# Kernel optimization log

Measured on AMD Instinct MI355X. Metric: run time of the kernel, lower is better.

Reference implementation:

```python
import jax, jax.numpy as jnp
import numpy as np
import math

D_EMBED = 128
NUM_HEADS = 4
HEAD_DIM = D_EMBED // NUM_HEADS


def setup_inputs() -> dict:
    key = jax.random.key(0)
    k1, k2, k3 = jax.random.split(key, 3)
    x = jax.random.normal(k1, (4, D_EMBED, 64, 64), dtype=jnp.float32)
    # nn.Linear(d_embed, 3*d_embed): weight [3d, d], bias [3d]; store transposed for x @ W
    scale = 1.0 / math.sqrt(D_EMBED)
    W_qkv = jax.random.uniform(k2, (D_EMBED, 3 * D_EMBED), dtype=jnp.float32, minval=-scale, maxval=scale)
    b_qkv = jax.random.uniform(k3, (3 * D_EMBED,), dtype=jnp.float32, minval=-scale, maxval=scale)
    return {"x": x, "W_qkv": W_qkv, "b_qkv": b_qkv}


def reference(x, W_qkv, b_qkv):
    b, c, h, w = x.shape
    n = h * w
    hd = HEAD_DIM
    # (b, c, h, w) -> (b, n, c) tokens
    t = jnp.transpose(x.reshape(b, c, n), (0, 2, 1))
    qkv = t @ W_qkv + b_qkv  # (b, n, 3c)
    q, k, v = jnp.split(qkv, 3, axis=-1)
    # (b, n, c) -> (b, heads, n, hd)
    def to_heads(u):
        return jnp.transpose(u.reshape(b, n, NUM_HEADS, hd), (0, 2, 1, 3))
    q, k, v = to_heads(q), to_heads(k), to_heads(v)
    # full O(n^2) score matrix, as in the source
    scores = jnp.einsum('bhqd,bhkd->bhqk', q, k) / math.sqrt(hd)
    weights = jax.nn.softmax(scores, axis=-1)
    out = jnp.einsum('bhqk,bhkd->bhqd', weights, v)  # (b, heads, n, hd)
    # permute(0,2,1,3) -> (b, n, heads, hd), then raw reshape to input shape (as in source)
    out = jnp.transpose(out, (0, 2, 1, 3)).reshape(b, c, h, w)
    return out + x
```

## Files before the change

kernel.cpp:

```cpp
#include <hip/hip_runtime.h>
#include <hip/hip_bf16.h>

#define BB 4
#define CC 128
#define NN 4096
#define HH 4
#define HD 32
#define NTOK (BB*NN)

typedef float f32x4 __attribute__((ext_vector_type(4)));
typedef short bf16x8 __attribute__((ext_vector_type(8)));
typedef unsigned short u16;
typedef unsigned int u32;

__device__ __forceinline__ u16 f2bf(float f) {
    union { float f; u32 u; } v; v.f = f;
    u32 r = v.u + 0x7FFF + ((v.u >> 16) & 1);
    return (u16)(r >> 16);
}

__device__ __forceinline__ u32 cvtpk(float lo, float hi) {
    u32 r;
    asm("v_cvt_pk_bf16_f32 %0, %1, %2" : "=v"(r) : "v"(lo), "v"(hi));
    return r;
}

__global__ __launch_bounds__(256) void prep_kernel(const float* __restrict__ x,
                                                   const float* __restrict__ W,
                                                   u16* __restrict__ t_bf,
                                                   u16* __restrict__ Wt_bf) {
    __shared__ u16 tile[64][65];
    int blk = blockIdx.x;
    const float* src; u16* dst; int src_cols, dst_cols, r0, c0;
    if (blk < 512) {
        int b  = blk >> 7;
        int rem = blk & 127;
        int ct = rem >> 6;
        int nt = rem & 63;
        src = x + b * CC * NN;  src_cols = NN; r0 = ct * 64; c0 = nt * 64;
        dst = t_bf + b * NN * CC; dst_cols = CC;
    } else {
        int rem = blk - 512;
        int kt = rem / 6, nt = rem % 6;
        src = W; src_cols = 3 * CC; r0 = kt * 64; c0 = nt * 64;
        dst = Wt_bf; dst_cols = CC;
    }
    int t = threadIdx.x;
#pragma unroll
    for (int p = 0; p < 16; ++p) {
        int rl = p * 4 + (t >> 6);
        int cl = t & 63;
        tile[rl][cl] = f2bf(src[(r0 + rl) * src_cols + c0 + cl]);
    }
    __syncthreads();
#pragma unroll
    for (int p = 0; p < 16; ++p) {
        int cl = p * 4 + (t >> 6);
        int rl = t & 63;
        dst[(c0 + cl) * dst_cols + r0 + rl] = tile[rl][cl];
    }
}

__global__ __launch_bounds__(256, 2) void qkv_gemm(const u16* __restrict__ t_bf,
                                                   const u16* __restrict__ Wt_bf,
                                                   const float* __restrict__ bias,
                                                   u16* __restrict__ Qb,
                                                   u16* __restrict__ Kb,
                                                   u16* __restrict__ Vb) {
    __shared__ u16 Al[128 * 128];
    __shared__ u16 Bl[128 * 128];
    int mt = blockIdx.x;
    int nt = blockIdx.y;
    int t = threadIdx.x;

    {
        const uint4* srcA = (const uint4*)(t_bf + mt * 128 * 128);
        const uint4* srcB = (const uint4*)(Wt_bf + nt * 128 * 128);
#pragma unroll
        for (int p = 0; p < 8; ++p) {
            int cid = p * 256 + t;
            int row = cid >> 4, c16 = cid & 15;
            int sw = (c16 ^ (row & 7)) * 8;
            *(uint4*)(Al + row * 128 + sw) = srcA[cid];
            *(uint4*)(Bl + row * 128 + sw) = srcB[cid];
        }
    }
    __syncthreads();

    int w = t >> 6, l = t & 63;
    int wq = (w >> 1) * 64, wn = (w & 1) * 64;
    int lr = l & 15, lg = l >> 4;

    f32x4 acc[4][4];
#pragma unroll
    for (int mi = 0; mi < 4; ++mi)
#pragma unroll
        for (int ni = 0; ni < 4; ++ni)
            acc[mi][ni] = f32x4{0.f, 0.f, 0.f, 0.f};

#pragma unroll
    for (int kk = 0; kk < 4; ++kk) {
        bf16x8 a[4], bb[4];
        int c = kk * 4 + lg;
#pragma unroll
        for (int mi = 0; mi < 4; ++mi) {
            int R = wq + mi * 16 + lr;
            a[mi] = *(const bf16x8*)(Al + R * 128 + ((c ^ (R & 7)) * 8));
        }
#pragma unroll
        for (int ni = 0; ni < 4; ++ni) {
            int R = wn + ni * 16 + lr;
            bb[ni] = *(const bf16x8*)(Bl + R * 128 + ((c ^ (R & 7)) * 8));
        }
#pragma unroll
        for (int mi = 0; mi < 4; ++mi)
#pragma unroll
            for (int ni = 0; ni < 4; ++ni)
                acc[mi][ni] = __builtin_amdgcn_mfma_f32_16x16x32_bf16(a[mi], bb[ni], acc[mi][ni], 0, 0, 0);
    }

    int b = mt >> 5;
    int tok0 = (mt & 31) * 128 + wq;
    u16* outbuf = (nt == 0) ? Qb : (nt == 1 ? Kb : Vb);
    float qscale = (nt == 0) ? 0.17677669529663687f : 1.0f;
#pragma unroll
    for (int mi = 0; mi < 4; ++mi)
#pragma unroll
        for (int ni = 0; ni < 4; ++ni) {
            int ch = wn + ni * 16 + lr;
            float bv = bias[nt * 128 + ch];
            int hh = ch >> 5, d = ch & 31;
#pragma unroll
            for (int r = 0; r < 4; ++r) {
                int tok = tok0 + mi * 16 + lg * 4 + r;
                float val = (acc[mi][ni][r] + bv) * qscale;
                outbuf[((b * HH + hh) * NN + tok) * HD + d] = f2bf(val);
            }
        }
}

__global__ __launch_bounds__(256) void v_transpose(const u16* __restrict__ Vb,
                                                   u16* __restrict__ Vtb) {
    __shared__ u16 tile[32][65];
    int bh = blockIdx.y;
    int i0 = blockIdx.x * 64;
    int t = threadIdx.x;
    {
        uint4 val = *(const uint4*)(Vb + (bh * NN + i0) * HD + t * 8);
        int row = t >> 2, d8 = (t & 3) * 8;
        u16 tmp[8]; *(uint4*)tmp = val;
#pragma unroll
        for (int j = 0; j < 8; ++j) tile[d8 + j][row] = tmp[j];
    }
    __syncthreads();
    {
        int d = t >> 3, i8 = (t & 7) * 8;
        u16 tmp[8];
#pragma unroll
        for (int j = 0; j < 8; ++j) tmp[j] = tile[d][i8 + j];
        *(uint4*)(Vtb + (bh * HD + d) * NN + i0 + i8) = *(uint4*)tmp;
    }
}

__global__ __launch_bounds__(512, 4) void attn_kernel(const u16* __restrict__ Qb,
                                                      const u16* __restrict__ Kb,
                                                      const u16* __restrict__ Vtb,
                                                      const float* __restrict__ x,
                                                      float* __restrict__ out) {
    __shared__ __align__(16) u16 smem[8192];
    u16* KL = smem;
    u16* VL = smem + 2048;

    int tid = threadIdx.x;
    int w = tid >> 6, l = tid & 63;
    int lr = l & 15, lg = l >> 4;
    int bh = blockIdx.y, b = bh >> 2, hh = bh & 3;
    int q0w = blockIdx.x * 128 + w * 16;

    bf16x8 qa = *(const bf16x8*)(Qb + ((size_t)bh * NN + q0w + lr) * HD + lg * 8);

    int kRow = tid >> 3, kOff = (tid & 7) * 4;
    const u16* gK = Kb + ((size_t)bh * NN + kRow) * HD + kOff;
    u16* kDst = KL + kRow * 32 + kOff;
    int vD = tid >> 4, vC8 = tid & 15;
    const u16* gV = Vtb + ((size_t)bh * HD + vD) * NN + vC8 * 4;
    u16* vDst = VL + vD * 64 + ((vC8 ^ (vD & 15)) * 4);

    f32x4 acc0 = {0.f,0.f,0.f,0.f}, acc1 = {0.f,0.f,0.f,0.f};
    float m = -1e30f, ll = 0.f;
    const float L2E = 1.44269504f;
    union PB { u32 w4[4]; bf16x8 v; };

    for (int kt = 0; kt < 64; ++kt) {
        uint2 kreg = *(const uint2*)(gK + kt * 64 * HD);
        uint2 vreg = *(const uint2*)(gV + kt * 64);
        __syncthreads();
        *(uint2*)kDst = kreg;
        *(uint2*)vDst = vreg;
        __syncthreads();

        bf16x8 ka0 = *(const bf16x8*)(KL + (lr     ) * 32 + lg * 8);
        bf16x8 ka1 = *(const bf16x8*)(KL + (16 + lr) * 32 + lg * 8);
        bf16x8 ka2 = *(const bf16x8*)(KL + (32 + lr) * 32 + lg * 8);
        bf16x8 ka3 = *(const bf16x8*)(KL + (48 + lr) * 32 + lg * 8);
        f32x4 z = {0.f,0.f,0.f,0.f};
        f32x4 s0 = __builtin_amdgcn_mfma_f32_16x16x32_bf16(ka0, qa, z, 0, 0, 0);
        f32x4 s1 = __builtin_amdgcn_mfma_f32_16x16x32_bf16(ka1, qa, z, 0, 0, 0);
        f32x4 s2 = __builtin_amdgcn_mfma_f32_16x16x32_bf16(ka2, qa, z, 0, 0, 0);
        f32x4 s3 = __builtin_amdgcn_mfma_f32_16x16x32_bf16(ka3, qa, z, 0, 0, 0);

        float t0 = fmaxf(fmaxf(s0[0], s0[1]), fmaxf(s0[2], s0[3]));
        float t1 = fmaxf(fmaxf(s1[0], s1[1]), fmaxf(s1[2], s1[3]));
        float t2 = fmaxf(fmaxf(s2[0], s2[1]), fmaxf(s2[2], s2[3]));
        float t3 = fmaxf(fmaxf(s3[0], s3[1]), fmaxf(s3[2], s3[3]));
        float pmax = fmaxf(fmaxf(t0, t1), fmaxf(t2, t3));
        pmax = fmaxf(pmax, __shfl_xor(pmax, 16));
        pmax = fmaxf(pmax, __shfl_xor(pmax, 32));
        float mnew = fmaxf(m, pmax);
        float alpha = __builtin_amdgcn_exp2f((m - mnew) * L2E);
        m = mnew;
        float mm = m * L2E;
#define EXPX(vv) vv = __builtin_amdgcn_exp2f(__builtin_fmaf(vv, L2E, -mm))
        EXPX(s0[0]); EXPX(s0[1]); EXPX(s0[2]); EXPX(s0[3]);
        EXPX(s1[0]); EXPX(s1[1]); EXPX(s1[2]); EXPX(s1[3]);
        EXPX(s2[0]); EXPX(s2[1]); EXPX(s2[2]); EXPX(s2[3]);
        EXPX(s3[0]); EXPX(s3[1]); EXPX(s3[2]); EXPX(s3[3]);
#undef EXPX
        float psum = ((s0[0] + s0[1]) + (s0[2] + s0[3]))
                   + ((s1[0] + s1[1]) + (s1[2] + s1[3]))
                   + ((s2[0] + s2[1]) + (s2[2] + s2[3]))
                   + ((s3[0] + s3[1]) + (s3[2] + s3[3]));
        psum += __shfl_xor(psum, 16);
        psum += __shfl_xor(psum, 32);
        ll = ll * alpha + psum;
        acc0 *= alpha; acc1 *= alpha;

        PB p0, p1;
        p0.w4[0] = cvtpk(s0[0], s0[1]); p0.w4[1] = cvtpk(s0[2], s0[3]);
        p0.w4[2] = cvtpk(s1[0], s1[1]); p0.w4[3] = cvtpk(s1[2], s1[3]);
        p1.w4[0] = cvtpk(s2[0], s2[1]); p1.w4[1] = cvtpk(s2[2], s2[3]);
        p1.w4[2] = cvtpk(s3[0], s3[1]); p1.w4[3] = cvtpk(s3[2], s3[3]);

#pragma unroll
        for (int dt = 0; dt < 2; ++dt) {
            int dd = dt * 16 + lr;
#pragma unroll
            for (int ks = 0; ks < 2; ++ks) {
                uint2 a0 = *(const uint2*)(VL + dd * 64 + ((ks * 8 + lg)     ^ lr) * 4);
                uint2 a1 = *(const uint2*)(VL + dd * 64 + ((ks * 8 + 4 + lg) ^ lr) * 4);
                PB va;
                va.w4[0] = a0.x; va.w4[1] = a0.y; va.w4[2] = a1.x; va.w4[3] = a1.y;
                f32x4& ac = dt ? acc1 : acc0;
                ac = __builtin_amdgcn_mfma_f32_16x16x32_bf16(va.v, (ks ? p1 : p0).v, ac, 0, 0, 0);
            }
        }
    }
    __syncthreads();

    float inv = 1.0f / ll;
    acc0 *= inv; acc1 *= inv;

    float* OW = (float*)smem + w * 512;
    *(f32x4*)(OW + lr * 32 + ((lg    ) ^ (lr & 7)) * 4) = acc0;
    *(f32x4*)(OW + lr * 32 + ((4 + lg) ^ (lr & 7)) * 4) = acc1;
    int q = l & 15, part = l >> 4;
    f32x4 r0 = *(const f32x4*)(OW + q * 32 + ((2 * part    ) ^ (q & 7)) * 4);
    f32x4 r1 = *(const f32x4*)(OW + q * 32 + ((2 * part + 1) ^ (q & 7)) * 4);

    size_t gbase = ((size_t)b * NN + q0w + q) * CC + hh * 32 + part * 8;
    f32x4 x0 = *(const f32x4*)(x + gbase);
    f32x4 x1 = *(const f32x4*)(x + gbase + 4);
    *(f32x4*)(out + gbase)     = r0 + x0;
    *(f32x4*)(out + gbase + 4) = r1 + x1;
}

extern "C" void kernel_launch(void* const* d_in, const int* in_sizes, int n_in,
                              void* d_out, int out_size, void* d_ws, size_t ws_size,
                              hipStream_t stream) {
    const float* x   = (const float*)d_in[0];
    const float* W   = (const float*)d_in[1];
    const float* bia = (const float*)d_in[2];
    float* out = (float*)d_out;

    char* ws = (char*)d_ws;
    size_t off = 0;
    u16* t_bf  = (u16*)(ws + off); off += (size_t)NTOK * CC * 2;
    u16* Wt_bf = (u16*)(ws + off); off += (size_t)384 * 128 * 2;
    u16* Qb    = (u16*)(ws + off); off += (size_t)BB * HH * NN * HD * 2;
    u16* Kb    = (u16*)(ws + off); off += (size_t)BB * HH * NN * HD * 2;
    u16* Vb    = (u16*)(ws + off); off += (size_t)BB * HH * NN * HD * 2;
    u16* Vtb   = (u16*)(ws + off); off += (size_t)BB * HH * NN * HD * 2;

    hipLaunchKernelGGL(prep_kernel, dim3(524), dim3(256), 0, stream, x, W, t_bf, Wt_bf);
    hipLaunchKernelGGL(qkv_gemm, dim3(128, 3), dim3(256), 0, stream, t_bf, Wt_bf, bia, Qb, Kb, Vb);
    hipLaunchKernelGGL(v_transpose, dim3(64, 16), dim3(256), 0, stream, Vb, Vtb);
    hipLaunchKernelGGL(attn_kernel, dim3(32, 16), dim3(512), 0, stream, Qb, Kb, Vtb, x, out);
}
```

Measured before the change: 153.3 us.

## Fuse V transpose into QKV GEMM epilogue and reorder attention grid

The QKV GEMM epilogue now writes V directly in transposed (head-dim major) layout using 8-byte vector stores, which removes the separate v_transpose kernel launch and its extra read/write pass over V. The attention grid is also swapped so that blockIdx.x indexes batch-head and blockIdx.y the query tile. Consecutive blocks then cover different heads, which changes how K/V reuse falls across the cache. The transposed stores are strided by NN, so the writes may coalesce less well than the old path.

```diff
diff --git a/kernel.cpp b/kernel.cpp
--- a/kernel.cpp
+++ b/kernel.cpp
@@ -66,7 +66,7 @@
                                                    const float* __restrict__ bias,
                                                    u16* __restrict__ Qb,
                                                    u16* __restrict__ Kb,
-                                                   u16* __restrict__ Vb) {
+                                                   u16* __restrict__ Vtb) {
     __shared__ u16 Al[128 * 128];
     __shared__ u16 Bl[128 * 128];
     int mt = blockIdx.x;
@@ -121,44 +121,37 @@
 
     int b = mt >> 5;
     int tok0 = (mt & 31) * 128 + wq;
-    u16* outbuf = (nt == 0) ? Qb : (nt == 1 ? Kb : Vb);
-    float qscale = (nt == 0) ? 0.17677669529663687f : 1.0f;
-#pragma unroll
-    for (int mi = 0; mi < 4; ++mi)
-#pragma unroll
-        for (int ni = 0; ni < 4; ++ni) {
-            int ch = wn + ni * 16 + lr;
-            float bv = bias[nt * 128 + ch];
-            int hh = ch >> 5, d = ch & 31;
-#pragma unroll
-            for (int r = 0; r < 4; ++r) {
-                int tok = tok0 + mi * 16 + lg * 4 + r;
-                float val = (acc[mi][ni][r] + bv) * qscale;
-                outbuf[((b * HH + hh) * NN + tok) * HD + d] = f2bf(val);
+    if (nt == 2) {
+#pragma unroll
+        for (int mi = 0; mi < 4; ++mi)
+#pragma unroll
+            for (int ni = 0; ni < 4; ++ni) {
+                int ch = wn + ni * 16 + lr;
+                float bv = bias[256 + ch];
+                int hh = ch >> 5, d = ch & 31;
+                int tok = tok0 + mi * 16 + lg * 4;
+                u16 tmp[4];
+#pragma unroll
+                for (int r = 0; r < 4; ++r) tmp[r] = f2bf(acc[mi][ni][r] + bv);
+                *(uint2*)(Vtb + ((size_t)(b * HH + hh) * HD + d) * NN + tok) = *(uint2*)tmp;
             }
-        }
-}
-
-__global__ __launch_bounds__(256) void v_transpose(const u16* __restrict__ Vb,
-                                                   u16* __restrict__ Vtb) {
-    __shared__ u16 tile[32][65];
-    int bh = blockIdx.y;
-    int i0 = blockIdx.x * 64;
-    int t = threadIdx.x;
-    {
-        uint4 val = *(const uint4*)(Vb + (bh * NN + i0) * HD + t * 8);
-        int row = t >> 2, d8 = (t & 3) * 8;
-        u16 tmp[8]; *(uint4*)tmp = val;
-#pragma unroll
-        for (int j = 0; j < 8; ++j) tile[d8 + j][row] = tmp[j];
-    }
-    __syncthreads();
-    {
-        int d = t >> 3, i8 = (t & 7) * 8;
-        u16 tmp[8];
-#pragma unroll
-        for (int j = 0; j < 8; ++j) tmp[j] = tile[d][i8 + j];
-        *(uint4*)(Vtb + (bh * HD + d) * NN + i0 + i8) = *(uint4*)tmp;
+    } else {
+        u16* outbuf = (nt == 0) ? Qb : Kb;
+        float qscale = (nt == 0) ? 0.17677669529663687f : 1.0f;
+#pragma unroll
+        for (int mi = 0; mi < 4; ++mi)
+#pragma unroll
+            for (int ni = 0; ni < 4; ++ni) {
+                int ch = wn + ni * 16 + lr;
+                float bv = bias[nt * 128 + ch];
+                int hh = ch >> 5, d = ch & 31;
+#pragma unroll
+                for (int r = 0; r < 4; ++r) {
+                    int tok = tok0 + mi * 16 + lg * 4 + r;
+                    float val = (acc[mi][ni][r] + bv) * qscale;
+                    outbuf[((b * HH + hh) * NN + tok) * HD + d] = f2bf(val);
+                }
+            }
     }
 }
 
@@ -174,8 +167,10 @@
     int tid = threadIdx.x;
     int w = tid >> 6, l = tid & 63;
     int lr = l & 15, lg = l >> 4;
-    int bh = blockIdx.y, b = bh >> 2, hh = bh & 3;
-    int q0w = blockIdx.x * 128 + w * 16;
+    int bh = blockIdx.x;
+    int qt = blockIdx.y;
+    int b = bh >> 2, hh = bh & 3;
+    int q0w = qt * 128 + w * 16;
 
     bf16x8 qa = *(const bf16x8*)(Qb + ((size_t)bh * NN + q0w + lr) * HD + lg * 8);
 
@@ -192,7 +187,7 @@
     union PB { u32 w4[4]; bf16x8 v; };
 
     for (int kt = 0; kt < 64; ++kt) {
-        uint2 kreg = *(const uint2*)(gK + kt * 64 * HD);
+        uint2 kreg = *(const uint2*)(gK + (size_t)kt * 64 * HD);
         uint2 vreg = *(const uint2*)(gV + kt * 64);
         __syncthreads();
         *(uint2*)kDst = kreg;
@@ -288,11 +283,9 @@
     u16* Wt_bf = (u16*)(ws + off); off += (size_t)384 * 128 * 2;
     u16* Qb    = (u16*)(ws + off); off += (size_t)BB * HH * NN * HD * 2;
     u16* Kb    = (u16*)(ws + off); off += (size_t)BB * HH * NN * HD * 2;
-    u16* Vb    = (u16*)(ws + off); off += (size_t)BB * HH * NN * HD * 2;
     u16* Vtb   = (u16*)(ws + off); off += (size_t)BB * HH * NN * HD * 2;
 
     hipLaunchKernelGGL(prep_kernel, dim3(524), dim3(256), 0, stream, x, W, t_bf, Wt_bf);
-    hipLaunchKernelGGL(qkv_gemm, dim3(128, 3), dim3(256), 0, stream, t_bf, Wt_bf, bia, Qb, Kb, Vb);
-    hipLaunchKernelGGL(v_transpose, dim3(64, 16), dim3(256), 0, stream, Vb, Vtb);
-    hipLaunchKernelGGL(attn_kernel, dim3(32, 16), dim3(512), 0, stream, Qb, Kb, Vtb, x, out);
-}
+    hipLaunchKernelGGL(qkv_gemm, dim3(128, 3), dim3(256), 0, stream, t_bf, Wt_bf, bia, Qb, Kb, Vtb);
+    hipLaunchKernelGGL(attn_kernel, dim3(16, 32), dim3(512), 0, stream, Qb, Kb, Vtb, x, out);
+}
```

Result: faster. 149.1 us (-2.8%).
